# Performance work log

Measured on AMD Instinct MI355X. Metric: run time of the kernel, lower is better.

Reference implementation:

```python
import jax, jax.numpy as jnp
import numpy as np

NEG_INF = -1e9  # stand-in for -INF in masked_fill

def setup_inputs() -> dict:
    key = jax.random.key(0)
    kq, kk, kv, km = jax.random.split(key, 4)
    B, H, S, D = 4, 16, 2048, 128
    query = jax.random.normal(kq, (B, H, S, D), dtype=jnp.float32)
    k_ = jax.random.normal(kk, (B, H, S, D), dtype=jnp.float32)
    value = jax.random.normal(kv, (B, H, S, D), dtype=jnp.float32)
    mask = jax.random.randint(km, (B, 1, 1, S), 0, 2, dtype=jnp.int32)
    return {"query": query, "key": k_, "value": value, "mask": mask}

def reference(query, key, value, mask):
    # _score: dot-product score  [B,H,Sq,Sk]
    score = jnp.einsum("bhqd,bhkd->bhqk", query, key)
    # _probability_normalize: masked_fill(mask==0, -INF) then softmax over keys
    score = jnp.where(mask == 0, NEG_INF, score)
    probability = jax.nn.softmax(score, axis=-1)
    # _attention_aggregate: probability @ value -> [B,H,Sq,D]
    return jnp.einsum("bhqk,bhkd->bhqd", probability, value)
```

## Files before the change

kernel.cpp:

```cpp
#include <hip/hip_runtime.h>

typedef _Float16 f16;
typedef _Float16 f16x8 __attribute__((ext_vector_type(8)));
typedef _Float16 f16x4 __attribute__((ext_vector_type(4)));
typedef float f32x4 __attribute__((ext_vector_type(4)));
typedef float f32x16 __attribute__((ext_vector_type(16)));
typedef unsigned short ushort_t;
typedef unsigned int uint_t;

#define SEQ 2048
#define DIM 128
#define KVBLK 64
#define NTMAX (SEQ / KVBLK)
#define TILE_BYTES 16384

typedef __attribute__((address_space(3))) char lds_char;
typedef __attribute__((address_space(1))) const char glb_char;

__device__ __forceinline__ void gload16(const void* g, void* l) {
  __builtin_amdgcn_global_load_lds((glb_char*)g, (lds_char*)l, 16, 0, 0);
}

__global__ __launch_bounds__(64)
void scan_mask(const int* __restrict__ Mg, int* __restrict__ cidx, int* __restrict__ ncomp) {
  const int b = blockIdx.x;
  const int l = threadIdx.x;
  int m[32];
  int cnt = 0;
  const int* mp = Mg + (size_t)b * SEQ + l * 32;
#pragma unroll
  for (int j = 0; j < 32; ++j) { m[j] = mp[j]; cnt += (m[j] != 0) ? 1 : 0; }
  int inc = cnt;
  for (int ofs = 1; ofs < 64; ofs <<= 1) {
    int v = __shfl_up(inc, ofs);
    if (l >= ofs) inc += v;
  }
  int pos = inc - cnt;
  int* cp = cidx + (size_t)b * SEQ;
  for (int j = 0; j < 32; ++j)
    if (m[j] != 0) cp[pos++] = l * 32 + j;
  if (l == 63) ncomp[b] = inc;
}

__global__ __launch_bounds__(256)
void prep_k(const float* __restrict__ Kg, char* __restrict__ Kws,
            const int* __restrict__ cidx, const int* __restrict__ ncomp) {
  const int tid  = threadIdx.x;
  const int blk  = blockIdx.x;
  const int head = blk >> 5, t = blk & 31;
  const int b    = head >> 4;
  const int nc   = ncomp[b];
  if (t >= ((nc + 63) >> 6)) return;
  const float* hin = Kg + (size_t)head * SEQ * DIM;
  const int* cp = cidx + (size_t)b * SEQ;
  char* out = Kws + (size_t)blk * TILE_BYTES;
#pragma unroll
  for (int i = 0; i < 4; ++i) {
    int u = i * 256 + tid;
    int krow = u >> 4;
    int un   = u & 15;
    int kidx = t * 64 + krow;
    union { f16 h[8]; uint4 u4; } c;
    if (kidx < nc) {
      const float* p = hin + (size_t)cp[kidx] * DIM + un * 8;
      float4 a = *(const float4*)p;
      float4 bq = *(const float4*)(p + 4);
      c.h[0]=(f16)a.x;  c.h[1]=(f16)a.y;  c.h[2]=(f16)a.z;  c.h[3]=(f16)a.w;
      c.h[4]=(f16)bq.x; c.h[5]=(f16)bq.y; c.h[6]=(f16)bq.z; c.h[7]=(f16)bq.w;
    } else {
      c.u4 = uint4{0, 0, 0, 0};
    }
    *(uint4*)(out + krow * 256 + ((un ^ (krow & 15)) << 4)) = c.u4;
  }
}

__global__ __launch_bounds__(256)
void prep_v(const float* __restrict__ Vg, char* __restrict__ Vws,
            const int* __restrict__ cidx, const int* __restrict__ ncomp) {
  __shared__ ushort_t Vs[KVBLK * 133];
  const int tid  = threadIdx.x;
  const int blk  = blockIdx.x;
  const int head = blk >> 5, t = blk & 31;
  const int b    = head >> 4;
  const int nc   = ncomp[b];
  if (t >= ((nc + 63) >> 6)) return;
  const float* hin = Vg + (size_t)head * SEQ * DIM;
  const int* cp = cidx + (size_t)b * SEQ;
  char* out = Vws + (size_t)blk * TILE_BYTES;
#pragma unroll
  for (int i = 0; i < 4; ++i) {
    int u = i * 256 + tid;
    int k  = u >> 4;
    int d0 = (u & 15) * 8;
    int kidx = t * 64 + k;
    f16 h[8];
    if (kidx < nc) {
      const float* p = hin + (size_t)cp[kidx] * DIM + d0;
      float4 a = *(const float4*)p;
      float4 bq = *(const float4*)(p + 4);
      h[0]=(f16)a.x;  h[1]=(f16)a.y;  h[2]=(f16)a.z;  h[3]=(f16)a.w;
      h[4]=(f16)bq.x; h[5]=(f16)bq.y; h[6]=(f16)bq.z; h[7]=(f16)bq.w;
    } else {
#pragma unroll
      for (int j = 0; j < 8; ++j) h[j] = (f16)0.f;
    }
#pragma unroll
    for (int j = 0; j < 8; ++j)
      Vs[k * 133 + d0 + j] = __builtin_bit_cast(ushort_t, h[j]);
  }
  __syncthreads();
#pragma unroll
  for (int i = 0; i < 4; ++i) {
    int u = i * 256 + tid;
    int d  = u >> 3;
    int un = u & 7;
    union { f16 h[8]; uint4 u4; } c;
#pragma unroll
    for (int j = 0; j < 8; ++j)
      c.h[j] = __builtin_bit_cast(f16, Vs[(un * 8 + j) * 133 + d]);
    *(uint4*)(out + d * 128 + ((un ^ (d & 7)) << 4)) = c.u4;
  }
}

__global__ __launch_bounds__(512, 2)
void attn_main32(const float* __restrict__ Qg, const char* __restrict__ Kws,
                 const char* __restrict__ Vws, const int* __restrict__ ncomp,
                 float* __restrict__ Og) {
  __shared__ __align__(16) char Kb[2][TILE_BYTES];
  __shared__ __align__(16) char Vb[2][TILE_BYTES];

  const int tid  = threadIdx.x;
  const int lane = tid & 63;
  const int q32  = lane & 31;
  const int h    = lane >> 5;
  const int w    = tid >> 6;
  (void)w;

  const int bid  = blockIdx.x;
  const int head = (bid & 7) * 8 + (bid >> 6);
  const int qblk = (bid >> 3) & 7;
  const size_t hbase = (size_t)head * SEQ * DIM;
  const int bb = head >> 4;

  const int nc  = ncomp[bb];
  const int ntb = (nc + 63) >> 6;

  const char* ktb = Kws + ((size_t)(head * NTMAX) << 14);
  const char* vtb = Vws + ((size_t)(head * NTMAX) << 14);

  const int qrow = qblk * 256 + (tid >> 6) * 32 + q32;

  f16x8 qf[8];
  {
    const float* qp = Qg + hbase + (size_t)qrow * DIM + h * 8;
#pragma unroll
    for (int c = 0; c < 8; ++c) {
      float4 a = *(const float4*)(qp + c * 16);
      float4 b = *(const float4*)(qp + c * 16 + 4);
      f16x8 f;
      f[0]=(f16)a.x; f[1]=(f16)a.y; f[2]=(f16)a.z; f[3]=(f16)a.w;
      f[4]=(f16)b.x; f[5]=(f16)b.y; f[6]=(f16)b.z; f[7]=(f16)b.w;
      qf[c] = f;
    }
  }

  f32x16 oacc[4];
#pragma unroll
  for (int dvt = 0; dvt < 4; ++dvt) oacc[dvt] = (f32x16)(0.f);
  float mrow = -INFINITY, lrow = 0.f;

#pragma unroll
  for (int i = 0; i < 2; ++i) {
    int u = i * 512 + tid;
    gload16(ktb + u * 16, &Kb[0][u * 16]);
    gload16(vtb + u * 16, &Vb[0][u * 16]);
  }

  int cur = 0;
  for (int t = 0; t < ntb; ++t) {
    if (t + 1 < ntb) {
      const char* kt2 = ktb + ((size_t)(t + 1) << 14);
      const char* vt2 = vtb + ((size_t)(t + 1) << 14);
      const int nb = cur ^ 1;
#pragma unroll
      for (int i = 0; i < 2; ++i) {
        int u = i * 512 + tid;
        gload16(kt2 + u * 16, &Kb[nb][u * 16]);
        gload16(vt2 + u * 16, &Vb[nb][u * 16]);
      }
      asm volatile("s_waitcnt vmcnt(4)" ::: "memory");
    } else {
      asm volatile("s_waitcnt vmcnt(0)" ::: "memory");
    }
    __builtin_amdgcn_s_barrier();
    asm volatile("" ::: "memory");

    f32x16 s[2];
#pragma unroll
    for (int kt2 = 0; kt2 < 2; ++kt2) {
      const int kb = t * 64 + kt2 * 32;
      if (kb + 32 <= nc) {
        s[kt2] = (f32x16)(0.f);
      } else {
#pragma unroll
        for (int ri = 0; ri < 16; ++ri)
          s[kt2][ri] = (kb + (ri >> 2) * 8 + 4 * h + (ri & 3) < nc) ? 0.f : -1e9f;
      }
      const int krow = kt2 * 32 + q32;
      const int ksw  = krow & 15;
      __builtin_amdgcn_s_setprio(1);
#pragma unroll
      for (int c = 0; c < 8; ++c) {
        f16x8 kf = *(const f16x8*)(&Kb[cur][krow * 256 + (((2 * c + h) ^ ksw) << 4)]);
        s[kt2] = __builtin_amdgcn_mfma_f32_32x32x16_f16(kf, qf[c], s[kt2], 0, 0, 0);
      }
      __builtin_amdgcn_s_setprio(0);
    }

    float mx[16];
#pragma unroll
    for (int r = 0; r < 16; ++r) mx[r] = fmaxf(s[0][r], s[1][r]);
#pragma unroll
    for (int r = 0; r < 8; ++r) mx[r] = fmaxf(mx[r], mx[r + 8]);
#pragma unroll
    for (int r = 0; r < 4; ++r) mx[r] = fmaxf(mx[r], mx[r + 4]);
    float pmax = fmaxf(fmaxf(mx[0], mx[1]), fmaxf(mx[2], mx[3]));
    pmax = fmaxf(pmax, __shfl_xor(pmax, 32));

    if (!__all(pmax - mrow <= 8.f)) {
      float mnew = fmaxf(mrow, pmax);
      float scf = __expf(mrow - mnew);
#pragma unroll
      for (int dvt = 0; dvt < 4; ++dvt)
#pragma unroll
        for (int r = 0; r < 16; ++r) oacc[dvt][r] *= scf;
      lrow *= scf;
      mrow = mnew;
    }

    float ps[16];
#pragma unroll
    for (int r = 0; r < 16; ++r) {
      s[0][r] = __expf(s[0][r] - mrow);
      s[1][r] = __expf(s[1][r] - mrow);
      ps[r] = s[0][r] + s[1][r];
    }
#pragma unroll
    for (int r = 0; r < 8; ++r) ps[r] += ps[r + 8];
#pragma unroll
    for (int r = 0; r < 4; ++r) ps[r] += ps[r + 4];
    float psum = (ps[0] + ps[1]) + (ps[2] + ps[3]);
    psum += __shfl_xor(psum, 32);
    lrow += psum;

    uint_t pkA[2][4], pkB[2][4];
#pragma unroll
    for (int t2 = 0; t2 < 2; ++t2)
#pragma unroll
      for (int m = 0; m < 4; ++m) {
        pkA[t2][m] = __builtin_bit_cast(uint_t,
            __builtin_amdgcn_cvt_pkrtz(s[t2][4 * m + 0], s[t2][4 * m + 1]));
        pkB[t2][m] = __builtin_bit_cast(uint_t,
            __builtin_amdgcn_cvt_pkrtz(s[t2][4 * m + 2], s[t2][4 * m + 3]));
      }

#pragma unroll
    for (int ks = 0; ks < 4; ++ks) {
      const int sk = ks & 1, tt = ks >> 1;
      uint_t Ao = h ? pkA[tt][2 * sk + 1] : pkA[tt][2 * sk];
      uint_t Bo = h ? pkB[tt][2 * sk + 1] : pkB[tt][2 * sk];
      uint_t As = h ? pkA[tt][2 * sk]     : pkA[tt][2 * sk + 1];
      uint_t Bs = h ? pkB[tt][2 * sk]     : pkB[tt][2 * sk + 1];
      uint_t Ax = (uint_t)__shfl_xor((int)As, 32);
      uint_t Bx = (uint_t)__shfl_xor((int)Bs, 32);
      union { uint_t u[4]; f16x8 v; } pa;
      pa.u[0] = h ? Ax : Ao;
      pa.u[1] = h ? Bx : Bo;
      pa.u[2] = h ? Ao : Ax;
      pa.u[3] = h ? Bo : Bx;
      __builtin_amdgcn_s_setprio(1);
#pragma unroll
      for (int dvt = 0; dvt < 4; ++dvt) {
        const int dv = dvt * 32 + q32;
        f16x8 vf = *(const f16x8*)(&Vb[cur][dv * 128 + (((2 * ks + h) ^ (dv & 7)) << 4)]);
        oacc[dvt] = __builtin_amdgcn_mfma_f32_32x32x16_f16(vf, pa.v, oacc[dvt], 0, 0, 0);
      }
      __builtin_amdgcn_s_setprio(0);
    }

    asm volatile("" ::: "memory");
    __builtin_amdgcn_s_barrier();
    asm volatile("" ::: "memory");
    cur ^= 1;
  }

  const float inv = 1.0f / lrow;
  float* op = Og + hbase + (size_t)qrow * DIM;
#pragma unroll
  for (int dvt = 0; dvt < 4; ++dvt)
#pragma unroll
    for (int rq = 0; rq < 4; ++rq) {
      float4 o4;
      o4.x = oacc[dvt][4 * rq + 0] * inv;
      o4.y = oacc[dvt][4 * rq + 1] * inv;
      o4.z = oacc[dvt][4 * rq + 2] * inv;
      o4.w = oacc[dvt][4 * rq + 3] * inv;
      *(float4*)(op + dvt * 32 + rq * 8 + h * 4) = o4;
    }
}

#define QT 64
#define P_STRIDE 72
#define VT_STRIDE 76
typedef _Float16 f16x4_t __attribute__((ext_vector_type(4)));
__global__ __launch_bounds__(256, 2)
void attn_fwd_fb(const float* __restrict__ Qg, const float* __restrict__ Kg,
                 const float* __restrict__ Vg, const int* __restrict__ Mg,
                 float* __restrict__ Og) {
  __shared__ __align__(16) ushort_t K_lds[QT * DIM];
  __shared__ __align__(16) ushort_t Vt_lds[DIM * VT_STRIDE];
  __shared__ __align__(16) ushort_t P_lds[QT * P_STRIDE];
  __shared__ int M_lds[KVBLK];
  const int tid  = threadIdx.x;
  const int lane = tid & 63;
  const int w    = tid >> 6;
  const int li   = lane & 15;
  const int g    = lane >> 4;
  const int bid  = blockIdx.x;
  const int nid  = (bid & 7) * 256 + (bid >> 3);
  const int head = nid >> 5;
  const int qblk = nid & 31;
  const size_t hbase = (size_t)head * SEQ * DIM;
  const int bb = head >> 4;
  f16x8 qf[4];
  {
    const float* qp = Qg + hbase + (size_t)(qblk * QT + w * 16 + li) * DIM + g * 8;
#pragma unroll
    for (int d0 = 0; d0 < 4; ++d0) {
      float4 a = *(const float4*)(qp + d0 * 32);
      float4 b = *(const float4*)(qp + d0 * 32 + 4);
      f16x8 f;
      f[0]=(f16)a.x; f[1]=(f16)a.y; f[2]=(f16)a.z; f[3]=(f16)a.w;
      f[4]=(f16)b.x; f[5]=(f16)b.y; f[6]=(f16)b.z; f[7]=(f16)b.w;
      qf[d0] = f;
    }
  }
  float mrow[4], lrow[4];
  f32x4 oacc[8];
#pragma unroll
  for (int r = 0; r < 4; ++r) { mrow[r] = -INFINITY; lrow[r] = 0.f; }
#pragma unroll
  for (int dt = 0; dt < 8; ++dt) oacc[dt] = (f32x4)(0.f);
  for (int t = 0; t < NTMAX; ++t) {
    const int k0 = t * KVBLK;
    __syncthreads();
    {
      const float4* kgp = (const float4*)(Kg + hbase + (size_t)k0 * DIM);
#pragma unroll
      for (int rr = 0; rr < 8; ++rr) {
        int fi = rr * 256 + tid;
        int krow = fi >> 5;
        int d4 = fi & 31;
        float4 v = kgp[fi];
        union { f16 h[4]; uint2 u; } c;
        c.h[0]=(f16)v.x; c.h[1]=(f16)v.y; c.h[2]=(f16)v.z; c.h[3]=(f16)v.w;
        int off = krow * 256 + ((d4 * 8) ^ ((krow & 7) << 4));
        *(uint2*)((char*)K_lds + off) = c.u;
      }
    }
    {
      const float* vgp = Vg + hbase + (size_t)k0 * DIM;
#pragma unroll
      for (int rr = 0; rr < 16; ++rr) {
        int u = rr * 256 + tid;
        int d = u & 127;
        int k2 = (u >> 7) * 2;
        float v0 = vgp[(size_t)k2 * DIM + d];
        float v1 = vgp[(size_t)(k2 + 1) * DIM + d];
        union { f16 h[2]; unsigned int u32; } c;
        c.h[0]=(f16)v0; c.h[1]=(f16)v1;
        *(unsigned int*)(Vt_lds + d * VT_STRIDE + k2) = c.u32;
      }
    }
    if (tid < KVBLK) M_lds[tid] = Mg[(size_t)bb * SEQ + k0 + tid];
    __syncthreads();
    f32x4 sacc[4];
#pragma unroll
    for (int kt = 0; kt < 4; ++kt) sacc[kt] = (f32x4)(0.f);
#pragma unroll
    for (int kt = 0; kt < 4; ++kt) {
      const int krow = kt * 16 + li;
      const int swz = (krow & 7) << 4;
#pragma unroll
      for (int d0 = 0; d0 < 4; ++d0) {
        f16x8 kf = *(const f16x8*)((const char*)K_lds + krow * 256 + ((d0 * 64 + g * 16) ^ swz));
        sacc[kt] = __builtin_amdgcn_mfma_f32_16x16x32_f16(qf[d0], kf, sacc[kt], 0, 0, 0);
      }
    }
    float tmax[4] = {-INFINITY, -INFINITY, -INFINITY, -INFINITY};
#pragma unroll
    for (int kt = 0; kt < 4; ++kt) {
      const bool ok = (M_lds[kt * 16 + li] != 0);
#pragma unroll
      for (int r = 0; r < 4; ++r) {
        float sv = ok ? sacc[kt][r] : -1e9f;
        sacc[kt][r] = sv;
        tmax[r] = fmaxf(tmax[r], sv);
      }
    }
#pragma unroll
    for (int r = 0; r < 4; ++r) {
      tmax[r] = fmaxf(tmax[r], __shfl_xor(tmax[r], 1));
      tmax[r] = fmaxf(tmax[r], __shfl_xor(tmax[r], 2));
      tmax[r] = fmaxf(tmax[r], __shfl_xor(tmax[r], 4));
      tmax[r] = fmaxf(tmax[r], __shfl_xor(tmax[r], 8));
    }
    float sc[4], psum[4];
#pragma unroll
    for (int r = 0; r < 4; ++r) {
      float mnew = fmaxf(mrow[r], tmax[r]);
      sc[r] = __expf(mrow[r] - mnew);
      mrow[r] = mnew;
      psum[r] = 0.f;
    }
#pragma unroll
    for (int dt = 0; dt < 8; ++dt)
#pragma unroll
      for (int r = 0; r < 4; ++r) oacc[dt][r] *= sc[r];
#pragma unroll
    for (int kt = 0; kt < 4; ++kt) {
#pragma unroll
      for (int r = 0; r < 4; ++r) {
        float p = __expf(sacc[kt][r] - mrow[r]);
        psum[r] += p;
        P_lds[(w * 16 + g * 4 + r) * P_STRIDE + kt * 16 + li] =
            __builtin_bit_cast(ushort_t, (f16)p);
      }
    }
#pragma unroll
    for (int r = 0; r < 4; ++r) {
      psum[r] += __shfl_xor(psum[r], 1);
      psum[r] += __shfl_xor(psum[r], 2);
      psum[r] += __shfl_xor(psum[r], 4);
      psum[r] += __shfl_xor(psum[r], 8);
      lrow[r] = lrow[r] * sc[r] + psum[r];
    }
#pragma unroll
    for (int c = 0; c < 2; ++c) {
      f16x8 pa = *(const f16x8*)(P_lds + (w * 16 + li) * P_STRIDE + c * 32 + g * 8);
#pragma unroll
      for (int dt = 0; dt < 8; ++dt) {
        const ushort_t* vp = Vt_lds + (dt * 16 + li) * VT_STRIDE + c * 32 + g * 8;
        f16x4_t v0 = *(const f16x4_t*)vp;
        f16x4_t v1 = *(const f16x4_t*)(vp + 4);
        f16x8 vf;
        vf[0]=v0[0]; vf[1]=v0[1]; vf[2]=v0[2]; vf[3]=v0[3];
        vf[4]=v1[0]; vf[5]=v1[1]; vf[6]=v1[2]; vf[7]=v1[3];
        oacc[dt] = __builtin_amdgcn_mfma_f32_16x16x32_f16(pa, vf, oacc[dt], 0, 0, 0);
      }
    }
  }
#pragma unroll
  for (int r = 0; r < 4; ++r) {
    float inv = 1.0f / lrow[r];
    float* op = Og + hbase + (size_t)(qblk * QT + w * 16 + g * 4 + r) * DIM + li;
#pragma unroll
    for (int dt = 0; dt < 8; ++dt) op[dt * 16] = oacc[dt][r] * inv;
  }
}

extern "C" void kernel_launch(void* const* d_in, const int* in_sizes, int n_in,
                              void* d_out, int out_size, void* d_ws, size_t ws_size,
                              hipStream_t stream) {
  (void)in_sizes; (void)n_in; (void)out_size;
  const float* Q = (const float*)d_in[0];
  const float* K = (const float*)d_in[1];
  const float* V = (const float*)d_in[2];
  const int*   M = (const int*)d_in[3];
  float*       O = (float*)d_out;

  const size_t half = (size_t)2048 * TILE_BYTES;
  const size_t cidx_off  = 2 * half;
  const size_t ncomp_off = cidx_off + (size_t)4 * SEQ * sizeof(int);
  const size_t need = ncomp_off + 4 * sizeof(int);

  if (ws_size >= need) {
    char* Kws = (char*)d_ws;
    char* Vws = Kws + half;
    int*  cidx  = (int*)((char*)d_ws + cidx_off);
    int*  ncomp = (int*)((char*)d_ws + ncomp_off);
    scan_mask<<<dim3(4), dim3(64), 0, stream>>>(M, cidx, ncomp);
    prep_k<<<dim3(2048), dim3(256), 0, stream>>>(K, Kws, cidx, ncomp);
    prep_v<<<dim3(2048), dim3(256), 0, stream>>>(V, Vws, cidx, ncomp);
    attn_main32<<<dim3(512), dim3(512), 0, stream>>>(Q, Kws, Vws, ncomp, O);
  } else {
    attn_fwd_fb<<<dim3(2048), dim3(256), 0, stream>>>(Q, K, V, M, O);
  }
}
```

Baseline: 143.6 us.

## Software-pipeline PV of previous tile behind QK of current tile

Restructures the attention loop so the P·V MFMAs for tile t-1 run right after the QK MFMAs for tile t, before the softmax of tile t. The packed probabilities are carried across iterations in registers, and a final PV pass runs after the loop. V loads are shifted one stage later than K loads. The aim is to let the MFMA work overlap the exp/max/sum VALU work and hide load latency. In exchange it keeps extra live registers, and the last iteration issues a redundant K-tile load.

Result: no change. 142.0 us (-1.1%).

```diff
diff --git a/kernel.cpp b/kernel.cpp
--- a/kernel.cpp
+++ b/kernel.cpp
@@ -122,6 +122,34 @@
   }
 }
 
+__device__ __forceinline__ void pv_accum(const char* __restrict__ Vbuf,
+                                         const uint_t pkA[2][4], const uint_t pkB[2][4],
+                                         f32x16 oacc[4], int q32, int h) {
+#pragma unroll
+  for (int ks = 0; ks < 4; ++ks) {
+    const int sk = ks & 1, tt = ks >> 1;
+    uint_t Ao = h ? pkA[tt][2 * sk + 1] : pkA[tt][2 * sk];
+    uint_t Bo = h ? pkB[tt][2 * sk + 1] : pkB[tt][2 * sk];
+    uint_t As = h ? pkA[tt][2 * sk]     : pkA[tt][2 * sk + 1];
+    uint_t Bs = h ? pkB[tt][2 * sk]     : pkB[tt][2 * sk + 1];
+    uint_t Ax = (uint_t)__shfl_xor((int)As, 32);
+    uint_t Bx = (uint_t)__shfl_xor((int)Bs, 32);
+    union { uint_t u[4]; f16x8 v; } pa;
+    pa.u[0] = h ? Ax : Ao;
+    pa.u[1] = h ? Bx : Bo;
+    pa.u[2] = h ? Ao : Ax;
+    pa.u[3] = h ? Bo : Bx;
+    __builtin_amdgcn_s_setprio(1);
+#pragma unroll
+    for (int dvt = 0; dvt < 4; ++dvt) {
+      const int dv = dvt * 32 + q32;
+      f16x8 vf = *(const f16x8*)(&Vbuf[dv * 128 + (((2 * ks + h) ^ (dv & 7)) << 4)]);
+      oacc[dvt] = __builtin_amdgcn_mfma_f32_32x32x16_f16(vf, pa.v, oacc[dvt], 0, 0, 0);
+    }
+    __builtin_amdgcn_s_setprio(0);
+  }
+}
+
 __global__ __launch_bounds__(512, 2)
 void attn_main32(const float* __restrict__ Qg, const char* __restrict__ Kws,
                  const char* __restrict__ Vws, const int* __restrict__ ncomp,
@@ -133,8 +161,6 @@
   const int lane = tid & 63;
   const int q32  = lane & 31;
   const int h    = lane >> 5;
-  const int w    = tid >> 6;
-  (void)w;
 
   const int bid  = blockIdx.x;
   const int head = (bid & 7) * 8 + (bid >> 6);
@@ -169,129 +195,145 @@
   for (int dvt = 0; dvt < 4; ++dvt) oacc[dvt] = (f32x16)(0.f);
   float mrow = -INFINITY, lrow = 0.f;
 
+  uint_t pkPA[2][4], pkPB[2][4];
+#pragma unroll
+  for (int t2 = 0; t2 < 2; ++t2)
+#pragma unroll
+    for (int m = 0; m < 4; ++m) { pkPA[t2][m] = 0; pkPB[t2][m] = 0; }
+
 #pragma unroll
   for (int i = 0; i < 2; ++i) {
     int u = i * 512 + tid;
     gload16(ktb + u * 16, &Kb[0][u * 16]);
-    gload16(vtb + u * 16, &Vb[0][u * 16]);
   }
 
   int cur = 0;
   for (int t = 0; t < ntb; ++t) {
-    if (t + 1 < ntb) {
-      const char* kt2 = ktb + ((size_t)(t + 1) << 14);
-      const char* vt2 = vtb + ((size_t)(t + 1) << 14);
+    {
+      const int tn = (t + 1 == ntb) ? 0 : t + 1;
+      const char* kt2 = ktb + ((size_t)tn << 14);
+      const char* vt2 = vtb + ((size_t)t << 14);
       const int nb = cur ^ 1;
 #pragma unroll
       for (int i = 0; i < 2; ++i) {
         int u = i * 512 + tid;
         gload16(kt2 + u * 16, &Kb[nb][u * 16]);
-        gload16(vt2 + u * 16, &Vb[nb][u * 16]);
-      }
-      asm volatile("s_waitcnt vmcnt(4)" ::: "memory");
-    } else {
-      asm volatile("s_waitcnt vmcnt(0)" ::: "memory");
-    }
+      }
+#pragma unroll
+      for (int i = 0; i < 2; ++i) {
+        int u = i * 512 + tid;
+        gload16(vt2 + u * 16, &Vb[cur][u * 16]);
+      }
+    }
+    asm volatile("s_waitcnt vmcnt(4)" ::: "memory");
     __builtin_amdgcn_s_barrier();
     asm volatile("" ::: "memory");
 
-    f32x16 s[2];
-#pragma unroll
-    for (int kt2 = 0; kt2 < 2; ++kt2) {
-      const int kb = t * 64 + kt2 * 32;
-      if (kb + 32 <= nc) {
-        s[kt2] = (f32x16)(0.f);
+    f32x16 s0, s1;
+    {
+      const int kb0 = t * 64;
+      if (kb0 + 32 <= nc) {
+        s0 = (f32x16)(0.f);
       } else {
 #pragma unroll
         for (int ri = 0; ri < 16; ++ri)
-          s[kt2][ri] = (kb + (ri >> 2) * 8 + 4 * h + (ri & 3) < nc) ? 0.f : -1e9f;
-      }
-      const int krow = kt2 * 32 + q32;
-      const int ksw  = krow & 15;
+          s0[ri] = (kb0 + (ri >> 2) * 8 + 4 * h + (ri & 3) < nc) ? 0.f : -1e9f;
+      }
+      const int kb1 = t * 64 + 32;
+      if (kb1 + 32 <= nc) {
+        s1 = (f32x16)(0.f);
+      } else {
+#pragma unroll
+        for (int ri = 0; ri < 16; ++ri)
+          s1[ri] = (kb1 + (ri >> 2) * 8 + 4 * h + (ri & 3) < nc) ? 0.f : -1e9f;
+      }
       __builtin_amdgcn_s_setprio(1);
-#pragma unroll
-      for (int c = 0; c < 8; ++c) {
-        f16x8 kf = *(const f16x8*)(&Kb[cur][krow * 256 + (((2 * c + h) ^ ksw) << 4)]);
-        s[kt2] = __builtin_amdgcn_mfma_f32_32x32x16_f16(kf, qf[c], s[kt2], 0, 0, 0);
+      {
+        const int krow = q32;
+        const int ksw  = krow & 15;
+#pragma unroll
+        for (int c = 0; c < 8; ++c) {
+          f16x8 kf = *(const f16x8*)(&Kb[cur][krow * 256 + (((2 * c + h) ^ ksw) << 4)]);
+          s0 = __builtin_amdgcn_mfma_f32_32x32x16_f16(kf, qf[c], s0, 0, 0, 0);
+        }
+      }
+      {
+        const int krow = 32 + q32;
+        const int ksw  = krow & 15;
+#pragma unroll
+        for (int c = 0; c < 8; ++c) {
+          f16x8 kf = *(const f16x8*)(&Kb[cur][krow * 256 + (((2 * c + h) ^ ksw) << 4)]);
+          s1 = __builtin_amdgcn_mfma_f32_32x32x16_f16(kf, qf[c], s1, 0, 0, 0);
+        }
       }
       __builtin_amdgcn_s_setprio(0);
     }
 
-    float mx[16];
-#pragma unroll
-    for (int r = 0; r < 16; ++r) mx[r] = fmaxf(s[0][r], s[1][r]);
-#pragma unroll
-    for (int r = 0; r < 8; ++r) mx[r] = fmaxf(mx[r], mx[r + 8]);
-#pragma unroll
-    for (int r = 0; r < 4; ++r) mx[r] = fmaxf(mx[r], mx[r + 4]);
-    float pmax = fmaxf(fmaxf(mx[0], mx[1]), fmaxf(mx[2], mx[3]));
-    pmax = fmaxf(pmax, __shfl_xor(pmax, 32));
-
-    if (!__all(pmax - mrow <= 8.f)) {
-      float mnew = fmaxf(mrow, pmax);
-      float scf = __expf(mrow - mnew);
-#pragma unroll
-      for (int dvt = 0; dvt < 4; ++dvt)
-#pragma unroll
-        for (int r = 0; r < 16; ++r) oacc[dvt][r] *= scf;
-      lrow *= scf;
-      mrow = mnew;
-    }
-
-    float ps[16];
-#pragma unroll
-    for (int r = 0; r < 16; ++r) {
-      s[0][r] = __expf(s[0][r] - mrow);
-      s[1][r] = __expf(s[1][r] - mrow);
-      ps[r] = s[0][r] + s[1][r];
-    }
-#pragma unroll
-    for (int r = 0; r < 8; ++r) ps[r] += ps[r + 8];
-#pragma unroll
-    for (int r = 0; r < 4; ++r) ps[r] += ps[r + 4];
-    float psum = (ps[0] + ps[1]) + (ps[2] + ps[3]);
-    psum += __shfl_xor(psum, 32);
-    lrow += psum;
-
-    uint_t pkA[2][4], pkB[2][4];
-#pragma unroll
-    for (int t2 = 0; t2 < 2; ++t2)
+    if (t > 0) {
+      pv_accum(&Vb[cur ^ 1][0], pkPA, pkPB, oacc, q32, h);
+    }
+
+    {
+      float mx[16];
+#pragma unroll
+      for (int r = 0; r < 16; ++r) mx[r] = fmaxf(s0[r], s1[r]);
+#pragma unroll
+      for (int r = 0; r < 8; ++r) mx[r] = fmaxf(mx[r], mx[r + 8]);
+#pragma unroll
+      for (int r = 0; r < 4; ++r) mx[r] = fmaxf(mx[r], mx[r + 4]);
+      float pmax = fmaxf(fmaxf(mx[0], mx[1]), fmaxf(mx[2], mx[3]));
+      pmax = fmaxf(pmax, __shfl_xor(pmax, 32));
+
+      if (!__all(pmax - mrow <= 8.f)) {
+        float mnew = fmaxf(mrow, pmax);
+        float scf = __expf(mrow - mnew);
+#pragma unroll
+        for (int dvt = 0; dvt < 4; ++dvt)
+#pragma unroll
+          for (int r = 0; r < 16; ++r) oacc[dvt][r] *= scf;
+        lrow *= scf;
+        mrow = mnew;
+      }
+
+      float ps[16];
+#pragma unroll
+      for (int r = 0; r < 16; ++r) {
+        s0[r] = __expf(s0[r] - mrow);
+        s1[r] = __expf(s1[r] - mrow);
+        ps[r] = s0[r] + s1[r];
+      }
+#pragma unroll
+      for (int r = 0; r < 8; ++r) ps[r] += ps[r + 8];
+#pragma unroll
+      for (int r = 0; r < 4; ++r) ps[r] += ps[r + 4];
+      float psum = (ps[0] + ps[1]) + (ps[2] + ps[3]);
+      psum += __shfl_xor(psum, 32);
+      lrow += psum;
+
 #pragma unroll
       for (int m = 0; m < 4; ++m) {
-        pkA[t2][m] = __builtin_bit_cast(uint_t,
-            __builtin_amdgcn_cvt_pkrtz(s[t2][4 * m + 0], s[t2][4 * m + 1]));
-        pkB[t2][m] = __builtin_bit_cast(uint_t,
-            __builtin_amdgcn_cvt_pkrtz(s[t2][4 * m + 2], s[t2][4 * m + 3]));
-      }
-
-#pragma unroll
-    for (int ks = 0; ks < 4; ++ks) {
-      const int sk = ks & 1, tt = ks >> 1;
-      uint_t Ao = h ? pkA[tt][2 * sk + 1] : pkA[tt][2 * sk];
-      uint_t Bo = h ? pkB[tt][2 * sk + 1] : pkB[tt][2 * sk];
-      uint_t As = h ? pkA[tt][2 * sk]     : pkA[tt][2 * sk + 1];
-      uint_t Bs = h ? pkB[tt][2 * sk]     : pkB[tt][2 * sk + 1];
-      uint_t Ax = (uint_t)__shfl_xor((int)As, 32);
-      uint_t Bx = (uint_t)__shfl_xor((int)Bs, 32);
-      union { uint_t u[4]; f16x8 v; } pa;
-      pa.u[0] = h ? Ax : Ao;
-      pa.u[1] = h ? Bx : Bo;
-      pa.u[2] = h ? Ao : Ax;
-      pa.u[3] = h ? Bo : Bx;
-      __builtin_amdgcn_s_setprio(1);
-#pragma unroll
-      for (int dvt = 0; dvt < 4; ++dvt) {
-        const int dv = dvt * 32 + q32;
-        f16x8 vf = *(const f16x8*)(&Vb[cur][dv * 128 + (((2 * ks + h) ^ (dv & 7)) << 4)]);
-        oacc[dvt] = __builtin_amdgcn_mfma_f32_32x32x16_f16(vf, pa.v, oacc[dvt], 0, 0, 0);
-      }
-      __builtin_amdgcn_s_setprio(0);
+        pkPA[0][m] = __builtin_bit_cast(uint_t,
+            __builtin_amdgcn_cvt_pkrtz(s0[4 * m + 0], s0[4 * m + 1]));
+        pkPB[0][m] = __builtin_bit_cast(uint_t,
+            __builtin_amdgcn_cvt_pkrtz(s0[4 * m + 2], s0[4 * m + 3]));
+        pkPA[1][m] = __builtin_bit_cast(uint_t,
+            __builtin_amdgcn_cvt_pkrtz(s1[4 * m + 0], s1[4 * m + 1]));
+        pkPB[1][m] = __builtin_bit_cast(uint_t,
+            __builtin_amdgcn_cvt_pkrtz(s1[4 * m + 2], s1[4 * m + 3]));
+      }
     }
 
     asm volatile("" ::: "memory");
     __builtin_amdgcn_s_barrier();
     asm volatile("" ::: "memory");
     cur ^= 1;
+  }
+
+  asm volatile("s_waitcnt vmcnt(0)" ::: "memory");
+  __builtin_amdgcn_s_barrier();
+  asm volatile("" ::: "memory");
+  if (ntb > 0) {
+    pv_accum(&Vb[cur ^ 1][0], pkPA, pkPB, oacc, q32, h);
   }
 
   const float inv = 1.0f / lrow;
```
